# Kernel optimization log

Hardware: AMD Instinct MI355X
Metric: run time of the kernel (lower is better)

Reference implementation:

```python
import jax, jax.numpy as jnp
import numpy as np
from jax import lax

TEMPERATURE = 0.0005


def conv1d(x, w, b, pad):
    # x: [B, Cin, T], w: [Cout, Cin, K], b: [Cout]
    y = lax.conv_general_dilated(x, w, window_strides=(1,), padding=[(pad, pad)],
                                 dimension_numbers=('NCH', 'OIH', 'NCH'))
    return y + b[None, :, None]


def setup_inputs() -> dict:
    key = jax.random.key(0)
    ks = jax.random.split(key, 16)
    B, Cq, Ck, Ca, Tde, Ten = 32, 80, 512, 80, 2000, 400

    def xavier(k, shape):
        fan_in = shape[1] * (shape[2] if len(shape) > 2 else 1)
        fan_out = shape[0] * (shape[2] if len(shape) > 2 else 1)
        lim = float(np.sqrt(6.0 / (fan_in + fan_out)))
        return jax.random.uniform(k, shape, jnp.float32, -lim, lim)

    inp = {
        'queries': jax.random.normal(ks[0], (B, Cq, Tde), jnp.float32),
        'keys': jax.random.normal(ks[1], (B, Ck, Ten), jnp.float32),
        'mask': jnp.ones((B, 1, Ten), jnp.int32),
        # key_layer: Conv(512->1024,k3,p1) -> ReLU -> Conv(1024->80,k1)
        'kw1': xavier(ks[2], (Ck * 2, Ck, 3)), 'kb1': jnp.zeros((Ck * 2,), jnp.float32),
        'kw2': xavier(ks[3], (Ca, Ck * 2, 1)), 'kb2': jnp.zeros((Ca,), jnp.float32),
        # query_layer: Conv(80->160,k3,p1)->ReLU->Conv(160->80,k1)->ReLU->Conv(80->80,k1)
        'qw1': xavier(ks[4], (Cq * 2, Cq, 3)), 'qb1': jnp.zeros((Cq * 2,), jnp.float32),
        'qw2': xavier(ks[5], (Cq, Cq * 2, 1)), 'qb2': jnp.zeros((Cq,), jnp.float32),
        'qw3': xavier(ks[6], (Ca, Cq, 1)), 'qb3': jnp.zeros((Ca,), jnp.float32),
    }
    return inp


def reference(queries, keys, mask, kw1, kb1, kw2, kb2, qw1, qb1, qw2, qb2, qw3, qb3):
    # key path: conv3 -> relu -> conv1
    k = conv1d(jax.nn.relu(conv1d(keys, kw1, kb1, 1)), kw2, kb2, 0)          # [B,Ca,Ten]
    # query path: conv3 -> relu -> conv1 -> relu -> conv1
    q = conv1d(queries, qw1, qb1, 1)
    q = jax.nn.relu(conv1d(jax.nn.relu(q), qw2, qb2, 0))
    q = conv1d(q, qw3, qb3, 0)                                               # [B,Ca,Tde]

    # sum_c (q - k)^2 = |q|^2 + |k|^2 - 2 q.k  (avoids [B,C,Tde,Ten] intermediate)
    q2 = jnp.sum(q * q, axis=1)                      # [B,Tde]
    k2 = jnp.sum(k * k, axis=1)                      # [B,Ten]
    qk = jnp.einsum('bcd,bce->bde', q, k)            # [B,Tde,Ten]
    dist = q2[:, :, None] + k2[:, None, :] - 2.0 * qk
    attn_logp = (-TEMPERATURE * dist)[:, None]       # [B,1,Tde,Ten]

    # masked fill over encoder positions (softmax dim)
    m = mask.astype(bool)[:, :, None, :]             # [B,1,1,Ten]
    attn_logp = jnp.where(m, attn_logp, -jnp.inf)
    attn = jax.nn.softmax(attn_logp, axis=3)
    return attn, attn_logp
```

## Files before the change

### kernel.cpp

```cpp
#include <hip/hip_runtime.h>
#include <hip/hip_bf16.h>
#include <math.h>

#define NB 32
#define CK 512
#define C1 1024
#define CA 80
#define CQ 80
#define CQ2 160
#define TEN 400
#define TDE 2000
#define KDIM 1536
#define TPAD 448
#define TQP 2048

static constexpr float TEMP = 0.0005f;

typedef __attribute__((ext_vector_type(8))) short short8;
typedef __attribute__((ext_vector_type(4))) float f32x4;

__device__ inline short f2bf(float v) {
  __hip_bfloat16 h = __float2bfloat16(v);
  return *(short*)&h;
}

__global__ __launch_bounds__(256) void cvt_w1_kernel(
    const float* __restrict__ w1, short* __restrict__ w1bf) {
  int i = blockIdx.x * 256 + threadIdx.x;
  if (i < C1 * KDIM) w1bf[i] = f2bf(w1[i]);
}

__global__ __launch_bounds__(256) void cvt_pad_kernel(
    const float* __restrict__ src, short* __restrict__ dst,
    int M, int K, int Mp, int Kp) {
  int i = blockIdx.x * 256 + threadIdx.x;
  if (i >= Mp * Kp) return;
  int r = i / Kp, c = i - r * Kp;
  float v = (r < M && c < K) ? src[(size_t)r * K + c] : 0.f;
  dst[i] = f2bf(v);
}

__global__ __launch_bounds__(256) void im2col_kernel(
    const float* __restrict__ keys, short* __restrict__ BmatT) {
  const int t = blockIdx.x;
  const int b = blockIdx.y;
  const int tid = threadIdx.x;
  short* dst = BmatT + ((size_t)b * TPAD + t) * KDIM;
  #pragma unroll
  for (int i = 0; i < 6; ++i) {
    int k = tid + i * 256;
    int ci = k / 3;
    int dk = k - ci * 3;
    int ts = t + dk - 1;
    float v = (ts >= 0 && ts < TEN) ? keys[((size_t)b * CK + ci) * TEN + ts] : 0.f;
    dst[k] = f2bf(v);
  }
}

__global__ __launch_bounds__(256) void im2col_q_kernel(
    const float* __restrict__ queries, short* __restrict__ Bq) {
  const int t = blockIdx.x;
  const int b = blockIdx.y;
  const int k = threadIdx.x;
  float v = 0.f;
  if (t < TDE && k < 240) {
    int ci = k / 3, dk = k - ci * 3, ts = t + dk - 1;
    v = (ts >= 0 && ts < TDE) ? queries[((size_t)b * CQ + ci) * TDE + ts] : 0.f;
  }
  Bq[((size_t)b * TQP + t) * 256 + k] = f2bf(v);
}

__global__ __launch_bounds__(256) void kconv1_mfma_kernel(
    const short* __restrict__ w1bf, const short* __restrict__ BmatT,
    const float* __restrict__ b1, short* __restrict__ k1t) {
  __shared__ short A_lds[2048];
  __shared__ short B_lds[2048];
  const int co0 = blockIdx.x * 64;
  const int t0  = blockIdx.y * 64;
  const int b   = blockIdx.z;
  const int tid = threadIdx.x;
  const int l = tid & 63, w = tid >> 6;
  const int srow = tid >> 2, sslot = tid & 3;

  const char* gA = (const char*)(w1bf + (size_t)(co0 + srow) * KDIM + sslot * 8);
  const char* gB = (const char*)(BmatT + ((size_t)b * TPAD + t0 + srow) * KDIM + sslot * 8);
  const int wbyte = (srow * 64 + sslot * 16) ^ ((srow & 7) << 4);

  const int kslot = l >> 4;
  const int arow = w * 16 + (l & 15);
  const int abyte = (arow * 64 + kslot * 16) ^ ((arow & 7) << 4);
  int bbyte[4];
  #pragma unroll
  for (int g = 0; g < 4; ++g) {
    int brow = g * 16 + (l & 15);
    bbyte[g] = (brow * 64 + kslot * 16) ^ ((brow & 7) << 4);
  }

  f32x4 acc[4];
  #pragma unroll
  for (int g = 0; g < 4; ++g) acc[g] = (f32x4){0.f, 0.f, 0.f, 0.f};

  for (int kt = 0; kt < KDIM / 32; ++kt) {
    uint4 av = *(const uint4*)(gA + (size_t)kt * 64);
    uint4 bv = *(const uint4*)(gB + (size_t)kt * 64);
    __syncthreads();
    *(uint4*)((char*)A_lds + wbyte) = av;
    *(uint4*)((char*)B_lds + wbyte) = bv;
    __syncthreads();
    short8 a = *(const short8*)((const char*)A_lds + abyte);
    #pragma unroll
    for (int g = 0; g < 4; ++g) {
      short8 bb = *(const short8*)((const char*)B_lds + bbyte[g]);
      acc[g] = __builtin_amdgcn_mfma_f32_16x16x32_bf16(a, bb, acc[g], 0, 0, 0);
    }
  }
  #pragma unroll
  for (int g = 0; g < 4; ++g) {
    int t = t0 + g * 16 + (l & 15);
    if (t < TEN) {
      #pragma unroll
      for (int r = 0; r < 4; ++r) {
        int co = co0 + w * 16 + kslot * 4 + r;
        float v = acc[g][r] + b1[co];
        k1t[((size_t)b * TPAD + t) * C1 + co] = f2bf(v > 0.f ? v : 0.f);
      }
    }
  }
}

template <int MODE, bool RELU>
__global__ __launch_bounds__(256) void qgemm_kernel(
    const short* __restrict__ A, const short* __restrict__ B,
    const float* __restrict__ bias, void* __restrict__ outv,
    int M, int Kpad, int kiters, int Nvalid, int outCols,
    size_t bBatchStride, size_t outBatchStride, int outLD) {
  __shared__ short A_lds[2048];
  __shared__ short B_lds[2048];
  const int co0 = blockIdx.x * 64;
  const int t0  = blockIdx.y * 64;
  const int b   = blockIdx.z;
  const int tid = threadIdx.x;
  const int l = tid & 63, w = tid >> 6;
  const int srow = tid >> 2, sslot = tid & 3;

  const short* gA = A + (size_t)(co0 + srow) * Kpad + sslot * 8;
  const short* gB = B + (size_t)b * bBatchStride + (size_t)(t0 + srow) * Kpad + sslot * 8;
  const int wbyte = (srow * 64 + sslot * 16) ^ ((srow & 7) << 4);

  const int kslot = l >> 4;
  const int arow = w * 16 + (l & 15);
  const int abyte = (arow * 64 + kslot * 16) ^ ((arow & 7) << 4);
  int bbyte[4];
  #pragma unroll
  for (int g = 0; g < 4; ++g) {
    int brow = g * 16 + (l & 15);
    bbyte[g] = (brow * 64 + kslot * 16) ^ ((brow & 7) << 4);
  }

  f32x4 acc[4];
  #pragma unroll
  for (int g = 0; g < 4; ++g) acc[g] = (f32x4){0.f, 0.f, 0.f, 0.f};

  uint4 av = *(const uint4*)gA;
  uint4 bv = *(const uint4*)gB;
  for (int kt = 0; kt < kiters; ++kt) {
    __syncthreads();
    *(uint4*)((char*)A_lds + wbyte) = av;
    *(uint4*)((char*)B_lds + wbyte) = bv;
    __syncthreads();
    uint4 an = av, bn = bv;
    if (kt + 1 < kiters) {
      an = *(const uint4*)(gA + (kt + 1) * 32);
      bn = *(const uint4*)(gB + (kt + 1) * 32);
    }
    short8 a = *(const short8*)((const char*)A_lds + abyte);
    #pragma unroll
    for (int g = 0; g < 4; ++g) {
      short8 bb = *(const short8*)((const char*)B_lds + bbyte[g]);
      acc[g] = __builtin_amdgcn_mfma_f32_16x16x32_bf16(a, bb, acc[g], 0, 0, 0);
    }
    av = an; bv = bn;
  }

  #pragma unroll
  for (int g = 0; g < 4; ++g) {
    int t = t0 + g * 16 + (l & 15);
    if (t >= Nvalid) continue;
    #pragma unroll
    for (int r = 0; r < 4; ++r) {
      int co = co0 + w * 16 + kslot * 4 + r;
      if (MODE == 1) {
        if (co < outCols) {
          float v = 0.f;
          if (co < M) {
            v = acc[g][r] + bias[co];
            if (RELU) v = v > 0.f ? v : 0.f;
          }
          ((short*)outv)[(size_t)b * outBatchStride + (size_t)t * outLD + co] = f2bf(v);
        }
      } else {
        if (co < M) {
          float v = acc[g][r] + bias[co];
          if (RELU) v = v > 0.f ? v : 0.f;
          ((float*)outv)[(size_t)b * outBatchStride + (size_t)co * outLD + t] = v;
        }
      }
    }
  }
}

__global__ __launch_bounds__(256) void prep_attn_q_kernel(
    const float* __restrict__ q3, short* __restrict__ qA,
    float* __restrict__ q2) {
  __shared__ float sm[80][64];
  const int b = blockIdx.y;
  const int t0 = blockIdx.x * 64;
  const int tid = threadIdx.x;
  for (int idx = tid; idx < 80 * 64; idx += 256) {
    int a = idx >> 6, j = idx & 63;
    int t = t0 + j;
    sm[a][j] = (t < TDE) ? q3[((size_t)b * CA + a) * TDE + t] : 0.f;
  }
  __syncthreads();
  if (tid < 64) {
    float ss = 0.f;
    #pragma unroll 8
    for (int a = 0; a < 80; ++a) { float v = sm[a][tid]; ss += v * v; }
    q2[(size_t)b * TQP + t0 + tid] = ss;
  }
  for (int idx = tid; idx < 64 * 96; idx += 256) {
    int j = idx / 96, k = idx - j * 96;
    float v = (k < 80) ? sm[k][j] : 0.f;
    qA[((size_t)b * TQP + t0 + j) * 96 + k] = f2bf(v);
  }
}

__global__ __launch_bounds__(256) void prep_attn_k_kernel(
    const float* __restrict__ kfeat, short* __restrict__ kB,
    float* __restrict__ k2) {
  __shared__ float sm[80][64];
  const int b = blockIdx.y;
  const int s0 = blockIdx.x * 64;
  const int tid = threadIdx.x;
  for (int idx = tid; idx < 80 * 64; idx += 256) {
    int a = idx >> 6, j = idx & 63;
    int s = s0 + j;
    sm[a][j] = (s < TEN) ? kfeat[((size_t)b * CA + a) * TEN + s] : 0.f;
  }
  __syncthreads();
  if (tid < 64) {
    float ss = 0.f;
    #pragma unroll 8
    for (int a = 0; a < 80; ++a) { float v = sm[a][tid]; ss += v * v; }
    k2[(size_t)b * TPAD + s0 + tid] = ss;
  }
  for (int idx = tid; idx < 64 * 96; idx += 256) {
    int j = idx / 96, k = idx - j * 96;
    float v = (k < 80) ? sm[k][j] : 0.f;
    kB[((size_t)b * TPAD + s0 + j) * 96 + k] = f2bf(v);
  }
}

__global__ __launch_bounds__(256) void attn_fused_kernel(
    const short* __restrict__ qA, const short* __restrict__ kB,
    const float* __restrict__ q2, const float* __restrict__ k2,
    const int* __restrict__ mask, float* __restrict__ out_attn,
    float* __restrict__ out_logp) {
  __shared__ short A_lds[3][2048];
  __shared__ short B_lds[3][2560];
  __shared__ float k2LDS[400];
  __shared__ int mLDS[400];
  const int t0 = blockIdx.x * 64;
  const int b  = blockIdx.y;
  const int tid = threadIdx.x;
  const int l = tid & 63, w = tid >> 6;

  {
    const int arow_s = tid >> 2, aslot = tid & 3;
    const short* gA = qA + ((size_t)b * TQP + t0 + arow_s) * 96 + aslot * 8;
    #pragma unroll
    for (int p = 0; p < 3; ++p) {
      uint4 v = *(const uint4*)(gA + p * 32);
      *(uint4*)((char*)&A_lds[p][0] +
                ((arow_s * 64 + aslot * 16) ^ ((arow_s & 7) << 4))) = v;
    }
  }
  for (int idx = tid; idx < 400; idx += 256) {
    k2LDS[idx] = k2[(size_t)b * TPAD + idx];
    mLDS[idx] = mask[(size_t)b * TEN + idx];
  }

  const int kslot = l >> 4;
  const int arow = w * 16 + (l & 15);
  const int abyte = (arow * 64 + kslot * 16) ^ ((arow & 7) << 4);

  f32x4 acc[25];
  #pragma unroll
  for (int i = 0; i < 25; ++i) acc[i] = (f32x4){0.f, 0.f, 0.f, 0.f};

  __syncthreads();
  #pragma unroll
  for (int st = 0; st < 5; ++st) {
    for (int idx = tid; idx < 960; idx += 256) {
      int row = idx / 12, c = idx - row * 12;
      int panel = c >> 2, ps = c & 3;
      uint4 v = *(const uint4*)(kB + ((size_t)b * TPAD + st * 80 + row) * 96 + c * 8);
      *(uint4*)((char*)&B_lds[panel][0] +
                ((row * 64 + ps * 16) ^ ((row & 7) << 4))) = v;
    }
    __syncthreads();
    #pragma unroll
    for (int kt = 0; kt < 3; ++kt) {
      short8 a = *(const short8*)((const char*)&A_lds[kt][0] + abyte);
      #pragma unroll
      for (int f = 0; f < 5; ++f) {
        int brow = f * 16 + (l & 15);
        short8 bb = *(const short8*)((const char*)&B_lds[kt][0] +
                                     ((brow * 64 + kslot * 16) ^ ((brow & 7) << 4)));
        acc[st * 5 + f] =
            __builtin_amdgcn_mfma_f32_16x16x32_bf16(a, bb, acc[st * 5 + f], 0, 0, 0);
      }
    }
    __syncthreads();
  }

  int trow[4]; float q2v[4];
  #pragma unroll
  for (int r = 0; r < 4; ++r) {
    trow[r] = t0 + w * 16 + kslot * 4 + r;
    q2v[r] = q2[(size_t)b * TQP + trow[r]];
  }
  #pragma unroll
  for (int sf = 0; sf < 25; ++sf) {
    int s = sf * 16 + (l & 15);
    float k2v = k2LDS[s];
    bool mk = mLDS[s] != 0;
    #pragma unroll
    for (int r = 0; r < 4; ++r) {
      float lp = mk ? (-TEMP) * (q2v[r] + k2v - 2.f * acc[sf][r]) : -INFINITY;
      acc[sf][r] = lp;
    }
  }
  #pragma unroll
  for (int r = 0; r < 4; ++r) {
    if (trow[r] < TDE) {
      float* dst = out_logp + ((size_t)(b * TDE + trow[r])) * TEN + (l & 15);
      #pragma unroll
      for (int sf = 0; sf < 25; ++sf) dst[sf * 16] = acc[sf][r];
    }
  }
  float m[4];
  #pragma unroll
  for (int r = 0; r < 4; ++r) m[r] = -INFINITY;
  #pragma unroll
  for (int sf = 0; sf < 25; ++sf)
    #pragma unroll
    for (int r = 0; r < 4; ++r) m[r] = fmaxf(m[r], acc[sf][r]);
  #pragma unroll
  for (int o = 1; o < 16; o <<= 1)
    #pragma unroll
    for (int r = 0; r < 4; ++r) m[r] = fmaxf(m[r], __shfl_xor(m[r], o, 64));
  float sum[4] = {0.f, 0.f, 0.f, 0.f};
  #pragma unroll
  for (int sf = 0; sf < 25; ++sf)
    #pragma unroll
    for (int r = 0; r < 4; ++r) {
      float v = acc[sf][r];
      float e = (v != -INFINITY) ? __expf(v - m[r]) : 0.f;
      acc[sf][r] = e;
      sum[r] += e;
    }
  #pragma unroll
  for (int o = 1; o < 16; o <<= 1)
    #pragma unroll
    for (int r = 0; r < 4; ++r) sum[r] += __shfl_xor(sum[r], o, 64);
  float inv[4];
  #pragma unroll
  for (int r = 0; r < 4; ++r) inv[r] = 1.0f / sum[r];
  #pragma unroll
  for (int r = 0; r < 4; ++r) {
    if (trow[r] < TDE) {
      float* dst = out_attn + ((size_t)(b * TDE + trow[r])) * TEN + (l & 15);
      #pragma unroll
      for (int sf = 0; sf < 25; ++sf) dst[sf * 16] = acc[sf][r] * inv[r];
    }
  }
}

extern "C" void kernel_launch(void* const* d_in, const int* in_sizes, int n_in,
                              void* d_out, int out_size, void* d_ws, size_t ws_size,
                              hipStream_t stream) {
  const float* queries = (const float*)d_in[0];
  const float* keys    = (const float*)d_in[1];
  const int*   mask    = (const int*)d_in[2];
  const float* kw1 = (const float*)d_in[3];
  const float* kb1 = (const float*)d_in[4];
  const float* kw2 = (const float*)d_in[5];
  const float* kb2 = (const float*)d_in[6];
  const float* qw1 = (const float*)d_in[7];
  const float* qb1 = (const float*)d_in[8];
  const float* qw2 = (const float*)d_in[9];
  const float* qb2 = (const float*)d_in[10];
  const float* qw3 = (const float*)d_in[11];
  const float* qb3 = (const float*)d_in[12];
  float* out = (float*)d_out;

  char* ws = (char*)d_ws;
  short* BmatT = (short*)ws;
  short* w1bf  = (short*)(ws + 44040192);
  short* k1t   = (short*)(ws + 47185920);
  short* w2bf  = (short*)(ws + 76546048);
  short* w1q   = (short*)(ws + 76808192);
  short* w2q   = (short*)(ws + 76906496);
  short* w3q   = (short*)(ws + 76947456);
  short* Bq    = (short*)ws;
  short* q1bf  = (short*)(ws + 33554432);
  short* q2bf  = (short*)(ws + 54525952);
  float* q3    = (float*)ws;
  short* qA    = (short*)(ws + 20480000);
  float* q2n   = (float*)(ws + 33062912);
  short* kB    = (short*)(ws + 47185920);
  float* k2n   = (float*)(ws + 49938432);
  float* kfeat = (float*)(ws + 81920000);

  const long long HALF = 25600000LL;
  float* out_attn = out;
  float* out_logp = out + HALF;

  cvt_w1_kernel<<<dim3((C1 * KDIM + 255) / 256), dim3(256), 0, stream>>>(kw1, w1bf);
  im2col_kernel<<<dim3(TEN, NB), dim3(256), 0, stream>>>(keys, BmatT);
  kconv1_mfma_kernel<<<dim3(16, 7, NB), dim3(256), 0, stream>>>(w1bf, BmatT, kb1, k1t);
  cvt_pad_kernel<<<dim3((128 * 1024 + 255) / 256), dim3(256), 0, stream>>>(
      kw2, w2bf, CA, C1, 128, C1);
  qgemm_kernel<2, false><<<dim3(2, 7, NB), dim3(256), 0, stream>>>(
      w2bf, k1t, kb2, kfeat, CA, C1, 32, TEN, CA,
      (size_t)TPAD * C1, (size_t)CA * TEN, TEN);

  cvt_pad_kernel<<<dim3((192 * 256 + 255) / 256), dim3(256), 0, stream>>>(
      qw1, w1q, CQ2, 240, 192, 256);
  cvt_pad_kernel<<<dim3((128 * 160 + 255) / 256), dim3(256), 0, stream>>>(
      qw2, w2q, CA, CQ2, 128, 160);
  cvt_pad_kernel<<<dim3((128 * 96 + 255) / 256), dim3(256), 0, stream>>>(
      qw3, w3q, CA, CQ, 128, 96);
  im2col_q_kernel<<<dim3(TQP, NB), dim3(256), 0, stream>>>(queries, Bq);
  qgemm_kernel<1, true><<<dim3(3, TQP / 64, NB), dim3(256), 0, stream>>>(
      w1q, Bq, qb1, q1bf, CQ2, 256, 8, TDE, 160,
      (size_t)TQP * 256, (size_t)TQP * 160, 160);
  qgemm_kernel<1, true><<<dim3(2, TQP / 64, NB), dim3(256), 0, stream>>>(
      w2q, q1bf, qb2, q2bf, CA, 160, 5, TDE, 96,
      (size_t)TQP * 160, (size_t)TQP * 96, 96);
  qgemm_kernel<2, false><<<dim3(2, TQP / 64, NB), dim3(256), 0, stream>>>(
      w3q, q2bf, qb3, q3, CA, 96, 3, TDE, 80,
      (size_t)TQP * 96, (size_t)CA * TDE, TDE);

  prep_attn_q_kernel<<<dim3(TQP / 64, NB), dim3(256), 0, stream>>>(q3, qA, q2n);
  prep_attn_k_kernel<<<dim3(TPAD / 64, NB), dim3(256), 0, stream>>>(kfeat, kB, k2n);
  attn_fused_kernel<<<dim3(TQP / 64, NB), dim3(256), 0, stream>>>(
      qA, kB, q2n, k2n, mask, out_attn, out_logp);
}
```

Measured before the change: 395.2 us.

## Widen kconv1 tile to 128 channels and load tiles directly into LDS

The key conv1 GEMM now uses a 128x64 output tile per block, with each wave computing two 16-row A fragments so every B fragment is reused twice. Global-to-register-to-LDS staging is replaced by global_load_lds direct transfers. The per-lane global addresses are pre-permuted with an inverse swizzle so the existing XOR-swizzled LDS read pattern still holds. This halves the grid and raises accumulator register use. The loop is still single-buffered with two barriers per k-step, so load latency is not overlapped.

```diff
diff --git a/kernel.cpp b/kernel.cpp
--- a/kernel.cpp
+++ b/kernel.cpp
@@ -24,6 +24,12 @@
   return *(short*)&h;
 }
 
+__device__ inline void gload_lds16(const void* g, void* l) {
+  __builtin_amdgcn_global_load_lds(
+      (const __attribute__((address_space(1))) unsigned int*)g,
+      (__attribute__((address_space(3))) unsigned int*)l, 16, 0, 0);
+}
+
 __global__ __launch_bounds__(256) void cvt_w1_kernel(
     const float* __restrict__ w1, short* __restrict__ w1bf) {
   int i = blockIdx.x * 256 + threadIdx.x;
@@ -73,22 +79,48 @@
 __global__ __launch_bounds__(256) void kconv1_mfma_kernel(
     const short* __restrict__ w1bf, const short* __restrict__ BmatT,
     const float* __restrict__ b1, short* __restrict__ k1t) {
-  __shared__ short A_lds[2048];
+  __shared__ short A_lds[4096];
   __shared__ short B_lds[2048];
-  const int co0 = blockIdx.x * 64;
+  const int co0 = blockIdx.x * 128;
   const int t0  = blockIdx.y * 64;
   const int b   = blockIdx.z;
   const int tid = threadIdx.x;
   const int l = tid & 63, w = tid >> 6;
-  const int srow = tid >> 2, sslot = tid & 3;
-
-  const char* gA = (const char*)(w1bf + (size_t)(co0 + srow) * KDIM + sslot * 8);
-  const char* gB = (const char*)(BmatT + ((size_t)b * TPAD + t0 + srow) * KDIM + sslot * 8);
-  const int wbyte = (srow * 64 + sslot * 16) ^ ((srow & 7) << 4);
+
+  auto invswz = [](int Y) {
+    int X = Y;
+    X ^= ((Y >> 8) & 1) << 6;
+    X ^= ((Y >> 7) & 1) << 5;
+    X ^= (((Y >> 6) ^ (Y >> 8)) & 1) << 4;
+    return X;
+  };
+
+  const short* gA[2];
+  #pragma unroll
+  for (int c = 0; c < 2; ++c) {
+    int Y = (w * 2 + c) * 1024 + l * 16;
+    int X = invswz(Y);
+    int row = X >> 6, slot = (X >> 4) & 3;
+    gA[c] = w1bf + (size_t)(co0 + row) * KDIM + slot * 8;
+  }
+  const short* gB;
+  {
+    int Y = w * 1024 + l * 16;
+    int X = invswz(Y);
+    int row = X >> 6, slot = (X >> 4) & 3;
+    gB = BmatT + ((size_t)b * TPAD + t0 + row) * KDIM + slot * 8;
+  }
+  short* ldsA0 = &A_lds[(w * 2 + 0) * 512];
+  short* ldsA1 = &A_lds[(w * 2 + 1) * 512];
+  short* ldsB  = &B_lds[w * 512];
 
   const int kslot = l >> 4;
-  const int arow = w * 16 + (l & 15);
-  const int abyte = (arow * 64 + kslot * 16) ^ ((arow & 7) << 4);
+  int abyte[2];
+  #pragma unroll
+  for (int i = 0; i < 2; ++i) {
+    int arow = w * 32 + i * 16 + (l & 15);
+    abyte[i] = (arow * 64 + kslot * 16) ^ ((arow & 7) << 4);
+  }
   int bbyte[4];
   #pragma unroll
   for (int g = 0; g < 4; ++g) {
@@ -96,33 +128,40 @@
     bbyte[g] = (brow * 64 + kslot * 16) ^ ((brow & 7) << 4);
   }
 
-  f32x4 acc[4];
-  #pragma unroll
-  for (int g = 0; g < 4; ++g) acc[g] = (f32x4){0.f, 0.f, 0.f, 0.f};
+  f32x4 acc[2][4];
+  #pragma unroll
+  for (int i = 0; i < 2; ++i)
+    #pragma unroll
+    for (int g = 0; g < 4; ++g) acc[i][g] = (f32x4){0.f, 0.f, 0.f, 0.f};
 
   for (int kt = 0; kt < KDIM / 32; ++kt) {
-    uint4 av = *(const uint4*)(gA + (size_t)kt * 64);
-    uint4 bv = *(const uint4*)(gB + (size_t)kt * 64);
-    __syncthreads();
-    *(uint4*)((char*)A_lds + wbyte) = av;
-    *(uint4*)((char*)B_lds + wbyte) = bv;
-    __syncthreads();
-    short8 a = *(const short8*)((const char*)A_lds + abyte);
+    __syncthreads();
+    gload_lds16(gA[0] + kt * 32, ldsA0);
+    gload_lds16(gA[1] + kt * 32, ldsA1);
+    gload_lds16(gB + kt * 32, ldsB);
+    __syncthreads();
+    short8 a0 = *(const short8*)((const char*)A_lds + abyte[0]);
+    short8 a1 = *(const short8*)((const char*)A_lds + abyte[1]);
     #pragma unroll
     for (int g = 0; g < 4; ++g) {
       short8 bb = *(const short8*)((const char*)B_lds + bbyte[g]);
-      acc[g] = __builtin_amdgcn_mfma_f32_16x16x32_bf16(a, bb, acc[g], 0, 0, 0);
-    }
-  }
+      acc[0][g] = __builtin_amdgcn_mfma_f32_16x16x32_bf16(a0, bb, acc[0][g], 0, 0, 0);
+      acc[1][g] = __builtin_amdgcn_mfma_f32_16x16x32_bf16(a1, bb, acc[1][g], 0, 0, 0);
+    }
+  }
+
   #pragma unroll
   for (int g = 0; g < 4; ++g) {
     int t = t0 + g * 16 + (l & 15);
     if (t < TEN) {
       #pragma unroll
-      for (int r = 0; r < 4; ++r) {
-        int co = co0 + w * 16 + kslot * 4 + r;
-        float v = acc[g][r] + b1[co];
-        k1t[((size_t)b * TPAD + t) * C1 + co] = f2bf(v > 0.f ? v : 0.f);
+      for (int i = 0; i < 2; ++i) {
+        #pragma unroll
+        for (int r = 0; r < 4; ++r) {
+          int co = co0 + w * 32 + i * 16 + kslot * 4 + r;
+          float v = acc[i][g][r] + b1[co];
+          k1t[((size_t)b * TPAD + t) * C1 + co] = f2bf(v > 0.f ? v : 0.f);
+        }
       }
     }
   }
@@ -429,7 +468,7 @@
 
   cvt_w1_kernel<<<dim3((C1 * KDIM + 255) / 256), dim3(256), 0, stream>>>(kw1, w1bf);
   im2col_kernel<<<dim3(TEN, NB), dim3(256), 0, stream>>>(keys, BmatT);
-  kconv1_mfma_kernel<<<dim3(16, 7, NB), dim3(256), 0, stream>>>(w1bf, BmatT, kb1, k1t);
+  kconv1_mfma_kernel<<<dim3(8, 7, NB), dim3(256), 0, stream>>>(w1bf, BmatT, kb1, k1t);
   cvt_pad_kernel<<<dim3((128 * 1024 + 255) / 256), dim3(256), 0, stream>>>(
       kw2, w2bf, CA, C1, 128, C1);
   qgemm_kernel<2, false><<<dim3(2, 7, NB), dim3(256), 0, stream>>>(
```

Measured after the change: 380.0 us. 3.8% less time.
